# Kernel optimization log

Measured on AMD Instinct MI355X. Metric: run time of the kernel, lower is better.

The kernel has to match this reference:

```python
import jax, jax.numpy as jnp
import numpy as np

B, L, N, F = 8, 4096, 128, 128          # batch, pixels (64x64), memories, filters
H, DK, DV = 8, 16, 32                   # heads, key dim/head, value dim/head
TK, TV = H * DK, H * DV                 # total key depth 128, total value depth 256
BOT, FFN = 256, 2048                    # bottleneck (2*filters), feed-forward channels
EPS = 1e-3                              # keras BatchNormalization epsilon
INV = float(1.0 / np.sqrt(1.0 + EPS))   # inference BN with moving mean=0, var=1


def _bn_pair(k, shape):
    kg, kb = jax.random.split(k)
    gamma = jax.random.uniform(kg, shape, jnp.float32, 0.5, 1.5)
    beta = 0.1 * jax.random.normal(kb, shape, jnp.float32)
    return jnp.stack([gamma, beta])


def setup_inputs() -> dict:
    key = jax.random.key(0)
    ks = jax.random.split(key, 24)
    s = float(BOT) ** -0.5  # TruncatedNormal(stddev=bottleneck**-0.5) init for qkv convs
    return {
        "pixel_input": jax.random.normal(ks[0], (B, L, F), jnp.float32),
        "memory_input": jax.random.normal(ks[1], (B, N, F), jnp.float32),
        "W_mem1": 0.05 * jax.random.normal(ks[2], (F, BOT), jnp.float32),
        "bn_mem1": _bn_pair(ks[3], (BOT,)),
        "W_pix1": 0.05 * jax.random.normal(ks[4], (F, BOT), jnp.float32),
        "bn_pix1": _bn_pair(ks[5], (BOT,)),
        "W_mem_qkv": s * jax.random.normal(ks[6], (BOT, 2 * TK + TV), jnp.float32),
        "bn_mem_qkv": _bn_pair(ks[7], (2 * TK + TV,)),
        "W_pix_qkv": s * jax.random.normal(ks[8], (BOT, 2 * TK + TV), jnp.float32),
        "bn_pix_qkv": _bn_pair(ks[9], (2 * TK + TV,)),
        "bn_mem_sim": _bn_pair(ks[10], (H,)),
        "bn_mem_ret": _bn_pair(ks[11], (H, DV)),
        "bn_pix_sim": _bn_pair(ks[12], (H,)),
        "bn_pix_ret": _bn_pair(ks[13], (H, DV)),
        "W_mem3": 0.05 * jax.random.normal(ks[14], (TV, F), jnp.float32),
        "bn_mem3": _bn_pair(ks[15], (F,)),
        "W_pix3": 0.05 * jax.random.normal(ks[16], (TV, F), jnp.float32),
        "bn_pix3": _bn_pair(ks[17], (F,)),
        "W_ffn1": 0.05 * jax.random.normal(ks[18], (F, FFN), jnp.float32),
        "bn_ffn1": _bn_pair(ks[19], (FFN,)),
        "W_ffn2": 0.05 * jax.random.normal(ks[20], (FFN, F), jnp.float32),
        "bn_ffn2": _bn_pair(ks[21], (F,)),
    }


def _cbn(x, W, p, relu=False):
    """Conv1D (kernel=1) + inference BatchNorm over channels (+ optional relu)."""
    y = jnp.einsum('blc,cd->bld', x, W)
    y = y * (p[0] * INV) + p[1]
    return jax.nn.relu(y) if relu else y


def _heads(t, d):
    b, l, _ = t.shape  # [b, l, H*d] -> [b, H, l, d]
    return t.reshape(b, l, H, d).transpose(0, 2, 1, 3)


def reference(pixel_input, memory_input, W_mem1, bn_mem1, W_pix1, bn_pix1,
              W_mem_qkv, bn_mem_qkv, W_pix_qkv, bn_pix_qkv,
              bn_mem_sim, bn_mem_ret, bn_pix_sim, bn_pix_ret,
              W_mem3, bn_mem3, W_pix3, bn_pix3,
              W_ffn1, bn_ffn1, W_ffn2, bn_ffn2):
    # Bottleneck projections (conv1 + BN + relu)
    mem = _cbn(memory_input, W_mem1, bn_mem1, True)   # [B, N, BOT]
    pix = _cbn(pixel_input, W_pix1, bn_pix1, True)    # [B, L, BOT]

    # QKV projections (conv + BN, no activation)
    mqkv = _cbn(mem, W_mem_qkv, bn_mem_qkv)           # [B, N, 2*TK+TV]
    pqkv = _cbn(pix, W_pix_qkv, bn_pix_qkv)           # [B, L, 2*TK+TV]
    mq, mk, mv = mqkv[..., :TK], mqkv[..., TK:2 * TK], mqkv[..., 2 * TK:]
    pq, pk, pv = pqkv[..., :TK], pqkv[..., TK:2 * TK], pqkv[..., 2 * TK:]
    mq_h, mk_h = _heads(mq, DK), _heads(mk, DK)       # [B, H, N, DK]
    pq_h, pk_h = _heads(pq, DK), _heads(pk, DK)       # [B, H, L, DK]
    mv_h = mv.reshape(B, N, H, DV)                    # [B, N, H, DV]
    pv_h = pv.reshape(B, L, H, DV)                    # [B, L, H, DV]

    # Memory path: memory2pixel attention + memory self-attention share softmax
    k_cat = jnp.concatenate([pk_h, mk_h], axis=2)     # [B, H, L+N, DK]
    v_cat = jnp.concatenate([pv_h, mv_h], axis=1)     # [B, L+N, H, DV]
    logits = jnp.einsum('bhnd,bhmd->bhnm', mq_h, k_cat)
    logits = logits * (bn_mem_sim[0] * INV)[None, :, None, None] + bn_mem_sim[1][None, :, None, None]
    attn = jax.nn.softmax(logits, axis=-1)
    ret = jnp.einsum('bhnm,bmhd->bhnd', attn, v_cat)  # [B, H, N, DV]
    ret = ret * (bn_mem_ret[0] * INV)[None, :, None, :] + bn_mem_ret[1][None, :, None, :]
    ret = jax.nn.relu(ret).transpose(0, 2, 1, 3).reshape(B, N, TV)
    mem_out = jax.nn.relu(memory_input + _cbn(ret, W_mem3, bn_mem3))
    ffn = _cbn(mem_out, W_ffn1, bn_ffn1, True)
    mem_out = jax.nn.relu(mem_out + _cbn(ffn, W_ffn2, bn_ffn2))

    # Pixel path: pixel2memory feedback attention (sigmoid activation)
    plogits = jnp.einsum('bhld,bhnd->bhln', pq_h, mk_h)
    plogits = plogits * (bn_pix_sim[0] * INV)[None, :, None, None] + bn_pix_sim[1][None, :, None, None]
    pattn = jax.nn.sigmoid(plogits)
    pret = jnp.einsum('bhln,bnhd->bhld', pattn, mv_h)  # [B, H, L, DV]
    pret = pret * (bn_pix_ret[0] * INV)[None, :, None, :] + bn_pix_ret[1][None, :, None, :]
    pret = jax.nn.relu(pret).transpose(0, 2, 1, 3).reshape(B, L, TV)
    pix_out = jax.nn.relu(pixel_input + _cbn(pret, W_pix3, bn_pix3))

    return pix_out, mem_out
```

## Files before the change

kernel.cpp:

```cpp
#include <hip/hip_runtime.h>

typedef __attribute__((ext_vector_type(8))) short short8;
typedef __attribute__((ext_vector_type(4))) float floatx4;

#define INVC 0.9995003746877732f
#define MSPLIT 8

__device__ __forceinline__ unsigned short f2bf(float f) {
    union { float f; unsigned int u; } c; c.f = f;
    unsigned int r = c.u + 0x7fffu + ((c.u >> 16) & 1u);
    return (unsigned short)(r >> 16);
}
__device__ __forceinline__ float bf2f(unsigned short u) {
    union { unsigned int u; float f; } c; c.u = ((unsigned int)u) << 16;
    return c.f;
}
__device__ __forceinline__ void gld_lds16(const unsigned short* g, unsigned short* l) {
    __builtin_amdgcn_global_load_lds(
        (const __attribute__((address_space(1))) unsigned int*)g,
        (__attribute__((address_space(3))) unsigned int*)l, 16, 0, 0);
}
__device__ __forceinline__ int fidx(int row, int k) {
    return (k >> 5) * 512 + (row + 16 * ((k >> 3) & 3)) * 8 + (k & 7);
}

struct PrepPtrs {
    const float* src_pix;
    unsigned short* dst_pix;
    const float* W[8]; unsigned short* Wt[8];
};

__global__ __launch_bounds__(256) void prep_kernel(PrepPtrs P) {
    __shared__ float T[32][33];
    const int bid = blockIdx.x, t = threadIdx.x;
    if (bid < 4096) {
        int i = bid * 1024 + t * 4;
        float4 v = *(const float4*)(P.src_pix + i);
        unsigned long long pk = (unsigned long long)f2bf(v.x)
            | ((unsigned long long)f2bf(v.y) << 16)
            | ((unsigned long long)f2bf(v.z) << 32)
            | ((unsigned long long)f2bf(v.w) << 48);
        *(unsigned long long*)(P.dst_pix + i) = pk;
        return;
    }
    int rel = bid - 4096;
    const int KD[8]  = {128,128,256,256,256,256,128,2048};
    const int ND[8]  = {256,256,512,512,128,128,2048,128};
    const int CNT[8] = {32,32,128,128,32,32,256,256};
    int wi = 0;
    #pragma unroll
    for (int k = 0; k < 8; ++k) { if (rel >= CNT[k] && wi == k) { rel -= CNT[k]; wi = k + 1; } }
    const int K = KD[wi], N = ND[wi];
    const int ntn = N >> 5;
    const int tn = rel % ntn, tk = rel / ntn;
    const int n0 = tn * 32, k0 = tk * 32;
    const float* W = P.W[wi];
    unsigned short* Wt = P.Wt[wi];
    const int tx = t & 31, ty = t >> 5;
    #pragma unroll
    for (int i = 0; i < 4; ++i)
        T[ty + 8*i][tx] = W[(size_t)(k0 + ty + 8*i) * N + n0 + tx];
    __syncthreads();
    #pragma unroll
    for (int i = 0; i < 4; ++i)
        Wt[(size_t)(n0 + ty + 8*i) * K + k0 + tx] = f2bf(T[tx][ty + 8*i]);
}

__device__ __forceinline__ void gemm_body(
    const unsigned short* __restrict__ A,
    const unsigned short* __restrict__ Bt,
    const float* __restrict__ bnp,
    const float* __restrict__ residF,
    unsigned short* __restrict__ outB,
    float* __restrict__ outF,
    int K, int Nc, int do_relu, int row0, int col0,
    unsigned short* As, unsigned short* Bs)
{
    const int t = threadIdx.x;
    const int lane = t & 63, w = t >> 6;
    const int l15 = lane & 15, quad = lane >> 4;
    const int wr = w >> 1, wc = w & 1;

    floatx4 acc[4][4];
    #pragma unroll
    for (int i = 0; i < 4; ++i)
        #pragma unroll
        for (int j = 0; j < 4; ++j) acc[i][j] = (floatx4){0.f, 0.f, 0.f, 0.f};

    const unsigned short* gA0 = A  + (size_t)(row0 + w*16     + l15) * K + quad*8;
    const unsigned short* gA1 = A  + (size_t)(row0 + (w+4)*16 + l15) * K + quad*8;
    const unsigned short* gB0 = Bt + (size_t)(col0 + w*16     + l15) * K + quad*8;
    const unsigned short* gB1 = Bt + (size_t)(col0 + (w+4)*16 + l15) * K + quad*8;
    unsigned short* lA0 = &As[w * 512];
    unsigned short* lA1 = &As[(w + 4) * 512];
    unsigned short* lB0 = &Bs[w * 512];
    unsigned short* lB1 = &Bs[(w + 4) * 512];

    for (int k0 = 0; k0 < K; k0 += 32) {
        __syncthreads();
        gld_lds16(gA0 + k0, lA0);
        gld_lds16(gA1 + k0, lA1);
        gld_lds16(gB0 + k0, lB0);
        gld_lds16(gB1 + k0, lB1);
        __syncthreads();
        short8 a[4], b[4];
        #pragma unroll
        for (int mt = 0; mt < 4; ++mt) a[mt] = *(const short8*)&As[(wr*4 + mt)*512 + lane*8];
        #pragma unroll
        for (int nt = 0; nt < 4; ++nt) b[nt] = *(const short8*)&Bs[(wc*4 + nt)*512 + lane*8];
        #pragma unroll
        for (int mt = 0; mt < 4; ++mt)
            #pragma unroll
            for (int nt = 0; nt < 4; ++nt)
                acc[mt][nt] = __builtin_amdgcn_mfma_f32_16x16x32_bf16(a[mt], b[nt], acc[mt][nt], 0, 0, 0);
    }

    #pragma unroll
    for (int mt = 0; mt < 4; ++mt) {
        const int rowb = row0 + wr*64 + mt*16 + quad*4;
        #pragma unroll
        for (int nt = 0; nt < 4; ++nt) {
            const int col = col0 + wc*64 + nt*16 + l15;
            floatx4 v = acc[mt][nt];
            const float g  = bnp[col] * INVC;
            const float be = bnp[Nc + col];
            #pragma unroll
            for (int r = 0; r < 4; ++r) {
                size_t off = (size_t)(rowb + r) * Nc + col;
                float v1 = v[r] * g + be;
                if (residF) v1 += residF[off];
                if (do_relu) v1 = fmaxf(v1, 0.f);
                if (outB) outB[off] = f2bf(v1);
                if (outF) outF[off] = v1;
            }
        }
    }
}

__global__ __launch_bounds__(256, 4) void gemm_bf16(
    const unsigned short* __restrict__ A, const unsigned short* __restrict__ Bt,
    const float* __restrict__ bnp, unsigned short* __restrict__ outB,
    int K, int Nc)
{
    __shared__ unsigned short As[8 * 512];
    __shared__ unsigned short Bs[8 * 512];
    gemm_body(A, Bt, bnp, nullptr, outB, nullptr, K, Nc, 0,
              blockIdx.y * 128, blockIdx.x * 128, As, Bs);
}

__global__ __launch_bounds__(256) void k_pix1_memfused(
    const unsigned short* __restrict__ pixB, const unsigned short* __restrict__ Wt1,
    const float* __restrict__ bn_pix1, unsigned short* __restrict__ pixA,
    const float* __restrict__ memory_input,
    const unsigned short* __restrict__ Wt0, const float* __restrict__ bn1,
    const unsigned short* __restrict__ Wt2, const float* __restrict__ bnq,
    unsigned short* __restrict__ mqkv)
{
    __shared__ unsigned short As[8 * 512];
    __shared__ unsigned short Bs[8 * 512];
    const int bx = blockIdx.x;
    if (bx < 512) {
        gemm_body(pixB, Wt1, bn_pix1, nullptr, pixA, nullptr, 128, 256, 1,
                  (bx >> 1) * 128, (bx & 1) * 128, As, Bs);
        return;
    }
    unsigned short* A0 = As;
    unsigned short* A1 = Bs;
    const int t = threadIdx.x;
    const int lane = t & 63, w = t >> 6;
    const int l15 = lane & 15, quad = lane >> 4;
    const int g0 = (bx - 512) * 16;

    {
        const int row = t >> 4;
        const int c0 = (t & 15) * 8;
        const float* src = memory_input + (size_t)(g0 + row) * 128 + c0;
        float4 v0 = *(const float4*)src;
        float4 v1 = *(const float4*)(src + 4);
        float vv[8] = {v0.x, v0.y, v0.z, v0.w, v1.x, v1.y, v1.z, v1.w};
        #pragma unroll
        for (int e = 0; e < 8; ++e)
            A0[fidx(row, c0 + e)] = f2bf(vv[e]);
    }
    __syncthreads();

    #pragma unroll
    for (int i = 0; i < 4; ++i) {
        const int n0 = (w*4 + i) * 16;
        floatx4 acc = {0.f,0.f,0.f,0.f};
        #pragma unroll
        for (int kc = 0; kc < 4; ++kc) {
            short8 a = *(const short8*)&A0[kc*512 + lane*8];
            short8 bfr = *(const short8*)&Wt0[(size_t)(n0 + l15)*128 + kc*32 + quad*8];
            acc = __builtin_amdgcn_mfma_f32_16x16x32_bf16(a, bfr, acc, 0, 0, 0);
        }
        const int col = n0 + l15;
        const float g = bn1[col] * INVC, be = bn1[256 + col];
        #pragma unroll
        for (int r = 0; r < 4; ++r) {
            const int row = quad*4 + r;
            float v = fmaxf(acc[r]*g + be, 0.f);
            A1[fidx(row, col)] = f2bf(v);
        }
    }
    __syncthreads();

    #pragma unroll
    for (int i = 0; i < 8; ++i) {
        const int n0 = w*128 + i*16;
        floatx4 acc = {0.f,0.f,0.f,0.f};
        #pragma unroll
        for (int kc = 0; kc < 8; ++kc) {
            short8 a = *(const short8*)&A1[kc*512 + lane*8];
            short8 bfr = *(const short8*)&Wt2[(size_t)(n0 + l15)*256 + kc*32 + quad*8];
            acc = __builtin_amdgcn_mfma_f32_16x16x32_bf16(a, bfr, acc, 0, 0, 0);
        }
        const int col = n0 + l15;
        const float g = bnq[col] * INVC, be = bnq[512 + col];
        #pragma unroll
        for (int r = 0; r < 4; ++r) {
            const int row = quad*4 + r;
            mqkv[(size_t)(g0 + row)*512 + col] = f2bf(acc[r]*g + be);
        }
    }
}

__global__ __launch_bounds__(256) void k_attn(
    const unsigned short* __restrict__ pqkv,
    const unsigned short* __restrict__ mqkv,
    const float* __restrict__ bn_psim, const float* __restrict__ bn_pret,
    unsigned short* __restrict__ pret,
    const float* __restrict__ bn_msim,
    float* __restrict__ part_acc, float* __restrict__ part_ml)
{
    __shared__ unsigned short Qs[128][40];
    __shared__ unsigned short Ks[128][40];
    __shared__ unsigned short VsT[32][136];
    __shared__ unsigned short Ps[128][136];
    const int t = threadIdx.x;
    const int lane = t & 63, w = t >> 6;
    const int l15 = lane & 15, quad = lane >> 4;
    floatx4 z4 = {0.f, 0.f, 0.f, 0.f};

    if (blockIdx.x < 2048) {
        const int bx = blockIdx.x;
        const int lt = bx & 31, h = (bx >> 5) & 7, b = bx >> 8;
        const int l0 = lt * 128;
        const float simg = bn_psim[h] * INVC, simb = bn_psim[8 + h];
        {
            const int r = t >> 1, half = t & 1;
            uint4 zz = make_uint4(0u, 0u, 0u, 0u);
            const unsigned short* qsrc = pqkv + ((size_t)(b*4096 + l0 + r) << 9) + h*16 + half*8;
            *(uint4*)&Qs[r][half*8] = *(const uint4*)qsrc;
            *(uint4*)&Qs[r][16 + half*8] = zz;
            const unsigned short* ksrc = mqkv + ((size_t)(b*128 + r) << 9) + 128 + h*16 + half*8;
            *(uint4*)&Ks[r][half*8] = *(const uint4*)ksrc;
            *(uint4*)&Ks[r][16 + half*8] = zz;
            const unsigned short* vsrc = mqkv + ((size_t)(b*128 + r) << 9) + 256 + h*32 + half*16;
            uint4 va = *(const uint4*)vsrc;
            uint4 vb = *(const uint4*)(vsrc + 8);
            const int d0 = half * 16;
            VsT[d0+0][r] = (unsigned short)(va.x & 0xffffu); VsT[d0+1][r] = (unsigned short)(va.x >> 16);
            VsT[d0+2][r] = (unsigned short)(va.y & 0xffffu); VsT[d0+3][r] = (unsigned short)(va.y >> 16);
            VsT[d0+4][r] = (unsigned short)(va.z & 0xffffu); VsT[d0+5][r] = (unsigned short)(va.z >> 16);
            VsT[d0+6][r] = (unsigned short)(va.w & 0xffffu); VsT[d0+7][r] = (unsigned short)(va.w >> 16);
            VsT[d0+8][r] = (unsigned short)(vb.x & 0xffffu); VsT[d0+9][r] = (unsigned short)(vb.x >> 16);
            VsT[d0+10][r] = (unsigned short)(vb.y & 0xffffu); VsT[d0+11][r] = (unsigned short)(vb.y >> 16);
            VsT[d0+12][r] = (unsigned short)(vb.z & 0xffffu); VsT[d0+13][r] = (unsigned short)(vb.z >> 16);
            VsT[d0+14][r] = (unsigned short)(vb.w & 0xffffu); VsT[d0+15][r] = (unsigned short)(vb.w >> 16);
        }
        __syncthreads();
        #pragma unroll
        for (int half = 0; half < 2; ++half) {
            short8 aq = *(const short8*)&Qs[w*32 + half*16 + l15][quad*8];
            #pragma unroll
            for (int nt = 0; nt < 8; ++nt) {
                short8 bk = *(const short8*)&Ks[nt*16 + l15][quad*8];
                floatx4 s = __builtin_amdgcn_mfma_f32_16x16x32_bf16(aq, bk, z4, 0, 0, 0);
                const int rowb = w*32 + half*16 + quad*4;
                #pragma unroll
                for (int r = 0; r < 4; ++r) {
                    float x = s[r] * simg + simb;
                    float p = 1.f / (1.f + __expf(-x));
                    Ps[rowb + r][nt*16 + l15] = f2bf(p);
                }
            }
        }
        __syncthreads();
        #pragma unroll
        for (int half = 0; half < 2; ++half) {
            const int mrow = w*32 + half*16;
            #pragma unroll
            for (int dvt = 0; dvt < 2; ++dvt) {
                floatx4 acc = {0.f, 0.f, 0.f, 0.f};
                #pragma unroll
                for (int ks = 0; ks < 4; ++ks) {
                    short8 ap = *(const short8*)&Ps[mrow + l15][ks*32 + quad*8];
                    short8 bv = *(const short8*)&VsT[dvt*16 + l15][ks*32 + quad*8];
                    acc = __builtin_amdgcn_mfma_f32_16x16x32_bf16(ap, bv, acc, 0, 0, 0);
                }
                const int dv = dvt*16 + l15;
                const float g  = bn_pret[h*32 + dv] * INVC;
                const float be = bn_pret[256 + h*32 + dv];
                #pragma unroll
                for (int r = 0; r < 4; ++r) {
                    const int row = l0 + mrow + quad*4 + r;
                    float v = fmaxf(acc[r] * g + be, 0.f);
                    pret[((size_t)(b*4096 + row) << 8) + h*32 + dv] = f2bf(v);
                }
            }
        }
        return;
    }

    const int bxm = blockIdx.x - 2048;
    const int s = bxm & (MSPLIT-1), h = (bxm >> 3) & 7, b = bxm >> 6;
    const int bh = b*8 + h;
    const float simg = bn_msim[h] * INVC, simb = bn_msim[8 + h];
    const int c0  = (s == 0) ? 0 : (4*s + 1);
    const int cnt = (s == 0) ? 5 : 4;

    {
        const int r = t >> 1, half = t & 1;
        uint4 zz = make_uint4(0u, 0u, 0u, 0u);
        const unsigned short* qsrc = mqkv + ((size_t)(b*128 + r) << 9) + h*16 + half*8;
        *(uint4*)&Qs[r][half*8] = *(const uint4*)qsrc;
        *(uint4*)&Qs[r][16 + half*8] = zz;
    }

    float m_run[2][4], l_run[2][4];
    floatx4 accpv[2][2];
    #pragma unroll
    for (int i = 0; i < 2; ++i) {
        #pragma unroll
        for (int r = 0; r < 4; ++r) { m_run[i][r] = -1e30f; l_run[i][r] = 0.f; }
        accpv[i][0] = (floatx4){0.f,0.f,0.f,0.f};
        accpv[i][1] = (floatx4){0.f,0.f,0.f,0.f};
    }

    for (int ci = 0; ci < cnt; ++ci) {
        const int c = c0 + ci;
        __syncthreads();
        {
            const int r = t >> 1, half = t & 1;
            uint4 zz = make_uint4(0u, 0u, 0u, 0u);
            const unsigned short* base = (c < 32)
                ? (pqkv + ((size_t)(b*4096 + c*128 + r) << 9))
                : (mqkv + ((size_t)(b*128 + r) << 9));
            *(uint4*)&Ks[r][half*8] = *(const uint4*)(base + 128 + h*16 + half*8);
            *(uint4*)&Ks[r][16 + half*8] = zz;
            const unsigned short* vsrc = base + 256 + h*32 + half*16;
            uint4 va = *(const uint4*)vsrc;
            uint4 vb = *(const uint4*)(vsrc + 8);
            const int d0 = half * 16;
            VsT[d0+0][r] = (unsigned short)(va.x & 0xffffu); VsT[d0+1][r] = (unsigned short)(va.x >> 16);
            VsT[d0+2][r] = (unsigned short)(va.y & 0xffffu); VsT[d0+3][r] = (unsigned short)(va.y >> 16);
            VsT[d0+4][r] = (unsigned short)(va.z & 0xffffu); VsT[d0+5][r] = (unsigned short)(va.z >> 16);
            VsT[d0+6][r] = (unsigned short)(va.w & 0xffffu); VsT[d0+7][r] = (unsigned short)(va.w >> 16);
            VsT[d0+8][r] = (unsigned short)(vb.x & 0xffffu); VsT[d0+9][r] = (unsigned short)(vb.x >> 16);
            VsT[d0+10][r] = (unsigned short)(vb.y & 0xffffu); VsT[d0+11][r] = (unsigned short)(vb.y >> 16);
            VsT[d0+12][r] = (unsigned short)(vb.z & 0xffffu); VsT[d0+13][r] = (unsigned short)(vb.z >> 16);
            VsT[d0+14][r] = (unsigned short)(vb.w & 0xffffu); VsT[d0+15][r] = (unsigned short)(vb.w >> 16);
        }
        __syncthreads();

        #pragma unroll
        for (int half = 0; half < 2; ++half) {
            float sv[8][4];
            short8 aq = *(const short8*)&Qs[w*32 + half*16 + l15][quad*8];
            #pragma unroll
            for (int nt = 0; nt < 8; ++nt) {
                short8 bk = *(const short8*)&Ks[nt*16 + l15][quad*8];
                floatx4 sr4 = __builtin_amdgcn_mfma_f32_16x16x32_bf16(aq, bk, z4, 0, 0, 0);
                #pragma unroll
                for (int r = 0; r < 4; ++r) sv[nt][r] = sr4[r] * simg + simb;
            }
            const int rowb = w*32 + half*16 + quad*4;
            #pragma unroll
            for (int r = 0; r < 4; ++r) {
                float mx = sv[0][r];
                #pragma unroll
                for (int nt = 1; nt < 8; ++nt) mx = fmaxf(mx, sv[nt][r]);
                mx = fmaxf(mx, __shfl_xor(mx, 1));
                mx = fmaxf(mx, __shfl_xor(mx, 2));
                mx = fmaxf(mx, __shfl_xor(mx, 4));
                mx = fmaxf(mx, __shfl_xor(mx, 8));
                float newm  = fmaxf(m_run[half][r], mx);
                float alpha = __expf(m_run[half][r] - newm);
                m_run[half][r] = newm;
                float lsum = 0.f;
                #pragma unroll
                for (int nt = 0; nt < 8; ++nt) {
                    float p = __expf(sv[nt][r] - newm);
                    lsum += p;
                    Ps[rowb + r][nt*16 + l15] = f2bf(p);
                }
                lsum += __shfl_xor(lsum, 1);
                lsum += __shfl_xor(lsum, 2);
                lsum += __shfl_xor(lsum, 4);
                lsum += __shfl_xor(lsum, 8);
                l_run[half][r] = l_run[half][r] * alpha + lsum;
                accpv[half][0][r] *= alpha;
                accpv[half][1][r] *= alpha;
            }
            __syncthreads();
            const int mrow = w*32 + half*16;
            #pragma unroll
            for (int dvt = 0; dvt < 2; ++dvt) {
                floatx4 a = accpv[half][dvt];
                #pragma unroll
                for (int ks = 0; ks < 4; ++ks) {
                    short8 ap = *(const short8*)&Ps[mrow + l15][ks*32 + quad*8];
                    short8 bv = *(const short8*)&VsT[dvt*16 + l15][ks*32 + quad*8];
                    a = __builtin_amdgcn_mfma_f32_16x16x32_bf16(ap, bv, a, 0, 0, 0);
                }
                accpv[half][dvt] = a;
            }
        }
    }

    #pragma unroll
    for (int half = 0; half < 2; ++half) {
        const int rowb = w*32 + half*16 + quad*4;
        #pragma unroll
        for (int dvt = 0; dvt < 2; ++dvt) {
            const int dv = dvt*16 + l15;
            #pragma unroll
            for (int r = 0; r < 4; ++r)
                part_acc[((size_t)(bh*MSPLIT + s)*128 + rowb + r)*32 + dv] = accpv[half][dvt][r];
        }
        if (l15 == 0) {
            #pragma unroll
            for (int r = 0; r < 4; ++r) {
                size_t o = ((size_t)(bh*MSPLIT + s)*128 + rowb + r) * 2;
                part_ml[o]     = m_run[half][r];
                part_ml[o + 1] = l_run[half][r];
            }
        }
    }
}

__global__ __launch_bounds__(256) void k_pix3_combmem3(
    const unsigned short* __restrict__ pretB, const unsigned short* __restrict__ Wt5,
    const float* __restrict__ bn_pix3, const float* __restrict__ pixel_input,
    float* __restrict__ out_pix,
    const float* __restrict__ part_acc, const float* __restrict__ part_ml,
    const float* __restrict__ bn_ret,
    const unsigned short* __restrict__ Wt4, const float* __restrict__ bn3,
    const float* __restrict__ memory_input,
    unsigned short* __restrict__ moB)
{
    __shared__ unsigned short As[8 * 512];
    __shared__ unsigned short Bs[8 * 512];
    const int bx = blockIdx.x;
    if (bx < 256) {
        gemm_body(pretB, Wt5, bn_pix3, pixel_input, nullptr, out_pix, 256, 128, 1,
                  bx * 128, 0, As, Bs);
        return;
    }
    unsigned short* mretA = As;
    const int t = threadIdx.x;
    const int lane = t & 63, w = t >> 6;
    const int l15 = lane & 15, quad = lane >> 4;
    const int g0 = (bx - 256) * 16;
    const int b = g0 >> 7;
    const int nbase = g0 & 127;

    {
        const int row = t >> 4;
        const int c0 = (t & 15) * 16;
        const int h = c0 >> 5;
        const int n = nbase + row;
        const int bh = b*8 + h;
        float ms[MSPLIT], ls[MSPLIT], m_g = -1e30f;
        #pragma unroll
        for (int s = 0; s < MSPLIT; ++s) {
            size_t o = ((size_t)(bh*MSPLIT + s)*128 + n)*2;
            ms[s] = part_ml[o]; ls[s] = part_ml[o+1];
            m_g = fmaxf(m_g, ms[s]);
        }
        float l_g = 0.f;
        float og[16];
        #pragma unroll
        for (int e = 0; e < 16; ++e) og[e] = 0.f;
        #pragma unroll
        for (int s = 0; s < MSPLIT; ++s) {
            float wgt = __expf(ms[s] - m_g);
            l_g += ls[s] * wgt;
            const float* pa = part_acc + ((size_t)(bh*MSPLIT + s)*128 + n)*32 + (c0 & 31);
            #pragma unroll
            for (int e = 0; e < 16; e += 4) {
                float4 v = *(const float4*)(pa + e);
                og[e]   += v.x*wgt; og[e+1] += v.y*wgt;
                og[e+2] += v.z*wgt; og[e+3] += v.w*wgt;
            }
        }
        float invl = 1.f / l_g;
        #pragma unroll
        for (int e = 0; e < 16; ++e) {
            int col = c0 + e;
            int dv = col & 31;
            float v = og[e]*invl*(bn_ret[h*32+dv]*INVC) + bn_ret[256 + h*32 + dv];
            mretA[fidx(row, col)] = f2bf(fmaxf(v, 0.f));
        }
    }
    __syncthreads();

    #pragma unroll
    for (int i = 0; i < 2; ++i) {
        const int n0 = (w*2 + i) * 16;
        floatx4 acc = {0.f,0.f,0.f,0.f};
        #pragma unroll
        for (int kc = 0; kc < 8; ++kc) {
            short8 a = *(const short8*)&mretA[kc*512 + lane*8];
            short8 bfr = *(const short8*)&Wt4[(size_t)(n0 + l15)*256 + kc*32 + quad*8];
            acc = __builtin_amdgcn_mfma_f32_16x16x32_bf16(a, bfr, acc, 0, 0, 0);
        }
        const int col = n0 + l15;
        const float g = bn3[col]*INVC, be = bn3[128 + col];
        #pragma unroll
        for (int r = 0; r < 4; ++r) {
            const int row = quad*4 + r;
            float v = acc[r]*g + be + memory_input[(size_t)(g0 + row)*128 + col];
            moB[(size_t)(g0 + row)*128 + col] = f2bf(fmaxf(v, 0.f));
        }
    }
}

__global__ __launch_bounds__(1024) void k_ffn(
    const unsigned short* __restrict__ moB,
    const unsigned short* __restrict__ Wt6, const float* __restrict__ bnf1,
    const unsigned short* __restrict__ Wt7, const float* __restrict__ bnf2,
    float* __restrict__ out_mem)
{
    __shared__ unsigned short moA[4*512];
    __shared__ unsigned short fA[64*512];
    __shared__ floatx4 red[2][8][64];
    const int t = threadIdx.x;
    const int lane = t & 63, w = t >> 6;
    const int l15 = lane & 15, quad = lane >> 4;
    const int g0 = blockIdx.x * 16;

    if (t < 256) {
        const int row = t >> 4;
        const int c0 = (t & 15) * 8;
        uint4 v = *(const uint4*)(moB + (size_t)(g0 + row)*128 + c0);
        unsigned short e0 = (unsigned short)(v.x & 0xffffu), e1 = (unsigned short)(v.x >> 16);
        unsigned short e2 = (unsigned short)(v.y & 0xffffu), e3 = (unsigned short)(v.y >> 16);
        unsigned short e4 = (unsigned short)(v.z & 0xffffu), e5 = (unsigned short)(v.z >> 16);
        unsigned short e6 = (unsigned short)(v.w & 0xffffu), e7 = (unsigned short)(v.w >> 16);
        moA[fidx(row, c0+0)] = e0; moA[fidx(row, c0+1)] = e1;
        moA[fidx(row, c0+2)] = e2; moA[fidx(row, c0+3)] = e3;
        moA[fidx(row, c0+4)] = e4; moA[fidx(row, c0+5)] = e5;
        moA[fidx(row, c0+6)] = e6; moA[fidx(row, c0+7)] = e7;
    }
    __syncthreads();

    #pragma unroll
    for (int i = 0; i < 8; ++i) {
        const int n0 = (w*8 + i) * 16;
        floatx4 acc = {0.f,0.f,0.f,0.f};
        #pragma unroll
        for (int kc = 0; kc < 4; ++kc) {
            short8 a = *(const short8*)&moA[kc*512 + lane*8];
            short8 bfr = *(const short8*)&Wt6[(size_t)(n0 + l15)*128 + kc*32 + quad*8];
            acc = __builtin_amdgcn_mfma_f32_16x16x32_bf16(a, bfr, acc, 0, 0, 0);
        }
        const int col = n0 + l15;
        const float g = bnf1[col]*INVC, be = bnf1[2048 + col];
        #pragma unroll
        for (int r = 0; r < 4; ++r)
            fA[fidx(quad*4 + r, col)] = f2bf(fmaxf(acc[r]*g + be, 0.f));
    }
    __syncthreads();

    {
        const int ntile = w & 7, khalf = w >> 3;
        const int n0 = ntile * 16;
        floatx4 acc = {0.f,0.f,0.f,0.f};
        #pragma unroll 8
        for (int kc = 0; kc < 32; ++kc) {
            const int kcu = khalf*32 + kc;
            short8 a = *(const short8*)&fA[kcu*512 + lane*8];
            short8 bfr = *(const short8*)&Wt7[(size_t)(n0 + l15)*2048 + kcu*32 + quad*8];
            acc = __builtin_amdgcn_mfma_f32_16x16x32_bf16(a, bfr, acc, 0, 0, 0);
        }
        red[khalf][ntile][lane] = acc;
    }
    __syncthreads();
    if (w < 8) {
        const int n0 = w * 16;
        floatx4 s0 = red[0][w][lane];
        floatx4 s1 = red[1][w][lane];
        const int col = n0 + l15;
        const float g = bnf2[col]*INVC, be = bnf2[128 + col];
        #pragma unroll
        for (int r = 0; r < 4; ++r) {
            const int row = quad*4 + r;
            float resid = bf2f(moA[fidx(row, col)]);
            float v = fmaxf((s0[r] + s1[r])*g + be + resid, 0.f);
            out_mem[(size_t)(g0 + row)*128 + col] = v;
        }
    }
}

extern "C" void kernel_launch(void* const* d_in, const int* in_sizes, int n_in,
                              void* d_out, int out_size, void* d_ws, size_t ws_size,
                              hipStream_t stream) {
    const float* pixel_input  = (const float*)d_in[0];
    const float* memory_input = (const float*)d_in[1];
    const float* W_mem1    = (const float*)d_in[2];
    const float* bn_mem1   = (const float*)d_in[3];
    const float* W_pix1    = (const float*)d_in[4];
    const float* bn_pix1   = (const float*)d_in[5];
    const float* W_mem_qkv = (const float*)d_in[6];
    const float* bn_mem_qkv= (const float*)d_in[7];
    const float* W_pix_qkv = (const float*)d_in[8];
    const float* bn_pix_qkv= (const float*)d_in[9];
    const float* bn_mem_sim= (const float*)d_in[10];
    const float* bn_mem_ret= (const float*)d_in[11];
    const float* bn_pix_sim= (const float*)d_in[12];
    const float* bn_pix_ret= (const float*)d_in[13];
    const float* W_mem3    = (const float*)d_in[14];
    const float* bn_mem3   = (const float*)d_in[15];
    const float* W_pix3    = (const float*)d_in[16];
    const float* bn_pix3   = (const float*)d_in[17];
    const float* W_ffn1    = (const float*)d_in[18];
    const float* bn_ffn1   = (const float*)d_in[19];
    const float* W_ffn2    = (const float*)d_in[20];
    const float* bn_ffn2   = (const float*)d_in[21];

    char* ws = (char*)d_ws;
    size_t off = 0;
    auto alloc = [&](size_t bytes) -> void* {
        void* p = ws + off; off += (bytes + 255) & ~(size_t)255; return p;
    };
    unsigned short* pixB  = (unsigned short*)alloc((size_t)32768*128*2);
    unsigned short* Wt0   = (unsigned short*)alloc((size_t)256*128*2);
    unsigned short* Wt1   = (unsigned short*)alloc((size_t)256*128*2);
    unsigned short* Wt2   = (unsigned short*)alloc((size_t)512*256*2);
    unsigned short* Wt3   = (unsigned short*)alloc((size_t)512*256*2);
    unsigned short* Wt4   = (unsigned short*)alloc((size_t)128*256*2);
    unsigned short* Wt5   = (unsigned short*)alloc((size_t)128*256*2);
    unsigned short* Wt6   = (unsigned short*)alloc((size_t)2048*128*2);
    unsigned short* Wt7   = (unsigned short*)alloc((size_t)128*2048*2);
    unsigned short* mqkvB = (unsigned short*)alloc((size_t)1024*512*2);
    unsigned short* pixA  = (unsigned short*)alloc((size_t)32768*256*2);
    unsigned short* pqkvB = (unsigned short*)alloc((size_t)32768*512*2);
    float* part_acc = (float*)alloc((size_t)64*MSPLIT*128*32*4);
    float* part_ml  = (float*)alloc((size_t)64*MSPLIT*128*2*4);
    unsigned short* pretB = (unsigned short*)alloc((size_t)32768*256*2);
    unsigned short* moB   = (unsigned short*)alloc((size_t)1024*128*2);

    float* out_pix = (float*)d_out;
    float* out_mem = (float*)d_out + (size_t)8*4096*128;

    PrepPtrs P;
    P.src_pix = pixel_input;
    P.dst_pix = pixB;
    P.W[0]=W_mem1; P.W[1]=W_pix1; P.W[2]=W_mem_qkv; P.W[3]=W_pix_qkv;
    P.W[4]=W_mem3; P.W[5]=W_pix3; P.W[6]=W_ffn1;    P.W[7]=W_ffn2;
    P.Wt[0]=Wt0; P.Wt[1]=Wt1; P.Wt[2]=Wt2; P.Wt[3]=Wt3;
    P.Wt[4]=Wt4; P.Wt[5]=Wt5; P.Wt[6]=Wt6; P.Wt[7]=Wt7;

    dim3 blk(256);
    prep_kernel<<<4992, blk, 0, stream>>>(P);
    k_pix1_memfused<<<576, blk, 0, stream>>>(pixB, Wt1, bn_pix1, pixA,
        memory_input, Wt0, bn_mem1, Wt2, bn_mem_qkv, mqkvB);
    gemm_bf16<<<dim3(4,256,1), blk, 0, stream>>>(pixA, Wt3, bn_pix_qkv, pqkvB, 256, 512);
    k_attn<<<2048 + 64*MSPLIT, blk, 0, stream>>>(pqkvB, mqkvB,
        bn_pix_sim, bn_pix_ret, pretB, bn_mem_sim, part_acc, part_ml);
    k_pix3_combmem3<<<320, blk, 0, stream>>>(pretB, Wt5, bn_pix3, pixel_input, out_pix,
        part_acc, part_ml, bn_mem_ret, Wt4, bn_mem3, memory_input, moB);
    k_ffn<<<64, dim3(1024), 0, stream>>>(moB, Wt6, bn_ffn1, Wt7, bn_ffn2, out_mem);
}
```

Baseline: 262.8 us.

## Split attention blocks finer and store LDS tiles in MFMA fragment layout

The attention kernel now uses 64-row query tiles, giving twice as many pixel blocks. The memory path moves from 8 splits, each looping over 4-5 chunks with an online softmax, to one block per (batch, head, query half, chunk) across 33 chunks, so each block handles a single chunk. Q, K, V-transpose and P tiles are stored in LDS in the MFMA fragment-contiguous layout so each lane reads with one short8 load, and launch bounds now request 4 blocks per CU. This spreads the work over more blocks and removes the serial chunk loop, but it grows the partial-result buffers and makes the combine stage loop over 33 partials instead of 8.

After: 264.3 us. About the same (+0.6%).

```diff
diff --git a/kernel.cpp b/kernel.cpp
--- a/kernel.cpp
+++ b/kernel.cpp
@@ -4,7 +4,7 @@
 typedef __attribute__((ext_vector_type(4))) float floatx4;
 
 #define INVC 0.9995003746877732f
-#define MSPLIT 8
+#define NCHUNK 33
 
 __device__ __forceinline__ unsigned short f2bf(float f) {
     union { float f; unsigned int u; } c; c.f = f;
@@ -225,7 +225,7 @@
     }
 }
 
-__global__ __launch_bounds__(256) void k_attn(
+__global__ __launch_bounds__(256, 4) void k_attn(
     const unsigned short* __restrict__ pqkv,
     const unsigned short* __restrict__ mqkv,
     const float* __restrict__ bn_psim, const float* __restrict__ bn_pret,
@@ -233,209 +233,160 @@
     const float* __restrict__ bn_msim,
     float* __restrict__ part_acc, float* __restrict__ part_ml)
 {
-    __shared__ unsigned short Qs[128][40];
-    __shared__ unsigned short Ks[128][40];
-    __shared__ unsigned short VsT[32][136];
-    __shared__ unsigned short Ps[128][136];
+    __shared__ unsigned short Qs[4*512];
+    __shared__ unsigned short Ks[8*512];
+    __shared__ unsigned short VsT[8*512];
+    __shared__ unsigned short Ps[16*512];
     const int t = threadIdx.x;
     const int lane = t & 63, w = t >> 6;
     const int l15 = lane & 15, quad = lane >> 4;
     floatx4 z4 = {0.f, 0.f, 0.f, 0.f};
-
-    if (blockIdx.x < 2048) {
+    const uint4 zz = make_uint4(0u,0u,0u,0u);
+
+    const int is_pix = (blockIdx.x < 4096);
+    int b, h, qrow0;
+    const unsigned short* kvbase;
+    if (is_pix) {
         const int bx = blockIdx.x;
-        const int lt = bx & 31, h = (bx >> 5) & 7, b = bx >> 8;
-        const int l0 = lt * 128;
-        const float simg = bn_psim[h] * INVC, simb = bn_psim[8 + h];
-        {
-            const int r = t >> 1, half = t & 1;
-            uint4 zz = make_uint4(0u, 0u, 0u, 0u);
-            const unsigned short* qsrc = pqkv + ((size_t)(b*4096 + l0 + r) << 9) + h*16 + half*8;
-            *(uint4*)&Qs[r][half*8] = *(const uint4*)qsrc;
-            *(uint4*)&Qs[r][16 + half*8] = zz;
-            const unsigned short* ksrc = mqkv + ((size_t)(b*128 + r) << 9) + 128 + h*16 + half*8;
-            *(uint4*)&Ks[r][half*8] = *(const uint4*)ksrc;
-            *(uint4*)&Ks[r][16 + half*8] = zz;
-            const unsigned short* vsrc = mqkv + ((size_t)(b*128 + r) << 9) + 256 + h*32 + half*16;
-            uint4 va = *(const uint4*)vsrc;
-            uint4 vb = *(const uint4*)(vsrc + 8);
-            const int d0 = half * 16;
-            VsT[d0+0][r] = (unsigned short)(va.x & 0xffffu); VsT[d0+1][r] = (unsigned short)(va.x >> 16);
-            VsT[d0+2][r] = (unsigned short)(va.y & 0xffffu); VsT[d0+3][r] = (unsigned short)(va.y >> 16);
-            VsT[d0+4][r] = (unsigned short)(va.z & 0xffffu); VsT[d0+5][r] = (unsigned short)(va.z >> 16);
-            VsT[d0+6][r] = (unsigned short)(va.w & 0xffffu); VsT[d0+7][r] = (unsigned short)(va.w >> 16);
-            VsT[d0+8][r] = (unsigned short)(vb.x & 0xffffu); VsT[d0+9][r] = (unsigned short)(vb.x >> 16);
-            VsT[d0+10][r] = (unsigned short)(vb.y & 0xffffu); VsT[d0+11][r] = (unsigned short)(vb.y >> 16);
-            VsT[d0+12][r] = (unsigned short)(vb.z & 0xffffu); VsT[d0+13][r] = (unsigned short)(vb.z >> 16);
-            VsT[d0+14][r] = (unsigned short)(vb.w & 0xffffu); VsT[d0+15][r] = (unsigned short)(vb.w >> 16);
-        }
-        __syncthreads();
-        #pragma unroll
-        for (int half = 0; half < 2; ++half) {
-            short8 aq = *(const short8*)&Qs[w*32 + half*16 + l15][quad*8];
-            #pragma unroll
-            for (int nt = 0; nt < 8; ++nt) {
-                short8 bk = *(const short8*)&Ks[nt*16 + l15][quad*8];
-                floatx4 s = __builtin_amdgcn_mfma_f32_16x16x32_bf16(aq, bk, z4, 0, 0, 0);
-                const int rowb = w*32 + half*16 + quad*4;
-                #pragma unroll
-                for (int r = 0; r < 4; ++r) {
-                    float x = s[r] * simg + simb;
-                    float p = 1.f / (1.f + __expf(-x));
-                    Ps[rowb + r][nt*16 + l15] = f2bf(p);
-                }
-            }
-        }
-        __syncthreads();
-        #pragma unroll
-        for (int half = 0; half < 2; ++half) {
-            const int mrow = w*32 + half*16;
-            #pragma unroll
-            for (int dvt = 0; dvt < 2; ++dvt) {
-                floatx4 acc = {0.f, 0.f, 0.f, 0.f};
-                #pragma unroll
-                for (int ks = 0; ks < 4; ++ks) {
-                    short8 ap = *(const short8*)&Ps[mrow + l15][ks*32 + quad*8];
-                    short8 bv = *(const short8*)&VsT[dvt*16 + l15][ks*32 + quad*8];
-                    acc = __builtin_amdgcn_mfma_f32_16x16x32_bf16(ap, bv, acc, 0, 0, 0);
-                }
-                const int dv = dvt*16 + l15;
-                const float g  = bn_pret[h*32 + dv] * INVC;
-                const float be = bn_pret[256 + h*32 + dv];
-                #pragma unroll
-                for (int r = 0; r < 4; ++r) {
-                    const int row = l0 + mrow + quad*4 + r;
-                    float v = fmaxf(acc[r] * g + be, 0.f);
-                    pret[((size_t)(b*4096 + row) << 8) + h*32 + dv] = f2bf(v);
-                }
-            }
-        }
-        return;
-    }
-
-    const int bxm = blockIdx.x - 2048;
-    const int s = bxm & (MSPLIT-1), h = (bxm >> 3) & 7, b = bxm >> 6;
-    const int bh = b*8 + h;
-    const float simg = bn_msim[h] * INVC, simb = bn_msim[8 + h];
-    const int c0  = (s == 0) ? 0 : (4*s + 1);
-    const int cnt = (s == 0) ? 5 : 4;
+        const int lt = bx & 63; h = (bx >> 6) & 7; b = bx >> 9;
+        qrow0 = b*4096 + lt*64;
+        kvbase = mqkv + ((size_t)(b*128) << 9);
+    } else {
+        const int bxm = blockIdx.x - 4096;
+        const int c = bxm % NCHUNK;
+        const int rest = bxm / NCHUNK;
+        const int qh = rest & 1; h = (rest >> 1) & 7; b = rest >> 4;
+        qrow0 = b*128 + qh*64;
+        kvbase = (c < 32) ? (pqkv + ((size_t)(b*4096 + c*128) << 9))
+                          : (mqkv + ((size_t)(b*128) << 9));
+    }
+    const unsigned short* qbase = is_pix ? pqkv : mqkv;
 
     {
         const int r = t >> 1, half = t & 1;
-        uint4 zz = make_uint4(0u, 0u, 0u, 0u);
-        const unsigned short* qsrc = mqkv + ((size_t)(b*128 + r) << 9) + h*16 + half*8;
-        *(uint4*)&Qs[r][half*8] = *(const uint4*)qsrc;
-        *(uint4*)&Qs[r][16 + half*8] = zz;
-    }
-
-    float m_run[2][4], l_run[2][4];
-    floatx4 accpv[2][2];
-    #pragma unroll
-    for (int i = 0; i < 2; ++i) {
-        #pragma unroll
-        for (int r = 0; r < 4; ++r) { m_run[i][r] = -1e30f; l_run[i][r] = 0.f; }
-        accpv[i][0] = (floatx4){0.f,0.f,0.f,0.f};
-        accpv[i][1] = (floatx4){0.f,0.f,0.f,0.f};
-    }
-
-    for (int ci = 0; ci < cnt; ++ci) {
-        const int c = c0 + ci;
-        __syncthreads();
-        {
-            const int r = t >> 1, half = t & 1;
-            uint4 zz = make_uint4(0u, 0u, 0u, 0u);
-            const unsigned short* base = (c < 32)
-                ? (pqkv + ((size_t)(b*4096 + c*128 + r) << 9))
-                : (mqkv + ((size_t)(b*128 + r) << 9));
-            *(uint4*)&Ks[r][half*8] = *(const uint4*)(base + 128 + h*16 + half*8);
-            *(uint4*)&Ks[r][16 + half*8] = zz;
-            const unsigned short* vsrc = base + 256 + h*32 + half*16;
-            uint4 va = *(const uint4*)vsrc;
-            uint4 vb = *(const uint4*)(vsrc + 8);
-            const int d0 = half * 16;
-            VsT[d0+0][r] = (unsigned short)(va.x & 0xffffu); VsT[d0+1][r] = (unsigned short)(va.x >> 16);
-            VsT[d0+2][r] = (unsigned short)(va.y & 0xffffu); VsT[d0+3][r] = (unsigned short)(va.y >> 16);
-            VsT[d0+4][r] = (unsigned short)(va.z & 0xffffu); VsT[d0+5][r] = (unsigned short)(va.z >> 16);
-            VsT[d0+6][r] = (unsigned short)(va.w & 0xffffu); VsT[d0+7][r] = (unsigned short)(va.w >> 16);
-            VsT[d0+8][r] = (unsigned short)(vb.x & 0xffffu); VsT[d0+9][r] = (unsigned short)(vb.x >> 16);
-            VsT[d0+10][r] = (unsigned short)(vb.y & 0xffffu); VsT[d0+11][r] = (unsigned short)(vb.y >> 16);
-            VsT[d0+12][r] = (unsigned short)(vb.z & 0xffffu); VsT[d0+13][r] = (unsigned short)(vb.z >> 16);
-            VsT[d0+14][r] = (unsigned short)(vb.w & 0xffffu); VsT[d0+15][r] = (unsigned short)(vb.w >> 16);
-        }
-        __syncthreads();
-
-        #pragma unroll
-        for (int half = 0; half < 2; ++half) {
-            float sv[8][4];
-            short8 aq = *(const short8*)&Qs[w*32 + half*16 + l15][quad*8];
+        if (t < 128) {
+            const unsigned short* src = qbase + ((size_t)(qrow0 + r) << 9) + h*16 + half*8;
+            *(uint4*)&Qs[(r>>4)*512 + ((r&15) + 16*half)*8] = *(const uint4*)src;
+            *(uint4*)&Qs[(r>>4)*512 + ((r&15) + 16*(2+half))*8] = zz;
+        }
+        const unsigned short* ksrc = kvbase + ((size_t)r << 9) + 128 + h*16 + half*8;
+        *(uint4*)&Ks[(r>>4)*512 + ((r&15) + 16*half)*8] = *(const uint4*)ksrc;
+        *(uint4*)&Ks[(r>>4)*512 + ((r&15) + 16*(2+half))*8] = zz;
+        const unsigned short* vsrc = kvbase + ((size_t)r << 9) + 256 + h*32 + half*16;
+        uint4 va = *(const uint4*)vsrc;
+        uint4 vb = *(const uint4*)(vsrc + 8);
+        unsigned short ev[16] = {
+            (unsigned short)(va.x & 0xffffu), (unsigned short)(va.x >> 16),
+            (unsigned short)(va.y & 0xffffu), (unsigned short)(va.y >> 16),
+            (unsigned short)(va.z & 0xffffu), (unsigned short)(va.z >> 16),
+            (unsigned short)(va.w & 0xffffu), (unsigned short)(va.w >> 16),
+            (unsigned short)(vb.x & 0xffffu), (unsigned short)(vb.x >> 16),
+            (unsigned short)(vb.y & 0xffffu), (unsigned short)(vb.y >> 16),
+            (unsigned short)(vb.z & 0xffffu), (unsigned short)(vb.z >> 16),
+            (unsigned short)(vb.w & 0xffffu), (unsigned short)(vb.w >> 16)};
+        const int vbase_off = (half*4 + (r>>5))*512 + 16*((r>>3)&3)*8 + (r&7);
+        #pragma unroll
+        for (int e = 0; e < 16; ++e)
+            VsT[vbase_off + e*8] = ev[e];
+    }
+    __syncthreads();
+
+    const float simg = (is_pix ? bn_psim[h] : bn_msim[h]) * INVC;
+    const float simb =  is_pix ? bn_psim[8 + h] : bn_msim[8 + h];
+    short8 aq = *(const short8*)&Qs[w*512 + lane*8];
+    float mx4[4], ls4[4];
+
+    if (is_pix) {
+        #pragma unroll
+        for (int nt = 0; nt < 8; ++nt) {
+            short8 bk = *(const short8*)&Ks[nt*512 + lane*8];
+            floatx4 s = __builtin_amdgcn_mfma_f32_16x16x32_bf16(aq, bk, z4, 0, 0, 0);
+            const int pbase = (w*4 + (nt>>1))*512 + 16*((nt&1)*2 + (l15>>3))*8 + (l15&7);
+            #pragma unroll
+            for (int r = 0; r < 4; ++r) {
+                float x = s[r] * simg + simb;
+                float p = __builtin_amdgcn_rcpf(1.f + __expf(-x));
+                Ps[pbase + (quad*4 + r)*8] = f2bf(p);
+            }
+        }
+    } else {
+        float sv[8][4];
+        #pragma unroll
+        for (int nt = 0; nt < 8; ++nt) {
+            short8 bk = *(const short8*)&Ks[nt*512 + lane*8];
+            floatx4 s = __builtin_amdgcn_mfma_f32_16x16x32_bf16(aq, bk, z4, 0, 0, 0);
+            #pragma unroll
+            for (int r = 0; r < 4; ++r) sv[nt][r] = s[r] * simg + simb;
+        }
+        #pragma unroll
+        for (int r = 0; r < 4; ++r) {
+            float mx = sv[0][r];
+            #pragma unroll
+            for (int nt = 1; nt < 8; ++nt) mx = fmaxf(mx, sv[nt][r]);
+            mx = fmaxf(mx, __shfl_xor(mx, 1));
+            mx = fmaxf(mx, __shfl_xor(mx, 2));
+            mx = fmaxf(mx, __shfl_xor(mx, 4));
+            mx = fmaxf(mx, __shfl_xor(mx, 8));
+            float lsum = 0.f;
             #pragma unroll
             for (int nt = 0; nt < 8; ++nt) {
-                short8 bk = *(const short8*)&Ks[nt*16 + l15][quad*8];
-                floatx4 sr4 = __builtin_amdgcn_mfma_f32_16x16x32_bf16(aq, bk, z4, 0, 0, 0);
-                #pragma unroll
-                for (int r = 0; r < 4; ++r) sv[nt][r] = sr4[r] * simg + simb;
+                float p = __expf(sv[nt][r] - mx);
+                lsum += p;
+                Ps[(w*4 + (nt>>1))*512 + ((quad*4+r) + 16*((nt&1)*2 + (l15>>3)))*8 + (l15&7)] = f2bf(p);
             }
-            const int rowb = w*32 + half*16 + quad*4;
+            lsum += __shfl_xor(lsum, 1);
+            lsum += __shfl_xor(lsum, 2);
+            lsum += __shfl_xor(lsum, 4);
+            lsum += __shfl_xor(lsum, 8);
+            mx4[r] = mx; ls4[r] = lsum;
+        }
+    }
+
+    #pragma unroll
+    for (int dvt = 0; dvt < 2; ++dvt) {
+        floatx4 acc = {0.f,0.f,0.f,0.f};
+        #pragma unroll
+        for (int ks = 0; ks < 4; ++ks) {
+            short8 ap = *(const short8*)&Ps[(w*4 + ks)*512 + lane*8];
+            short8 bv = *(const short8*)&VsT[(dvt*4 + ks)*512 + lane*8];
+            acc = __builtin_amdgcn_mfma_f32_16x16x32_bf16(ap, bv, acc, 0, 0, 0);
+        }
+        if (is_pix) {
+            const int dv = dvt*16 + l15;
+            const float g  = bn_pret[h*32 + dv] * INVC;
+            const float be = bn_pret[256 + h*32 + dv];
             #pragma unroll
             for (int r = 0; r < 4; ++r) {
-                float mx = sv[0][r];
-                #pragma unroll
-                for (int nt = 1; nt < 8; ++nt) mx = fmaxf(mx, sv[nt][r]);
-                mx = fmaxf(mx, __shfl_xor(mx, 1));
-                mx = fmaxf(mx, __shfl_xor(mx, 2));
-                mx = fmaxf(mx, __shfl_xor(mx, 4));
-                mx = fmaxf(mx, __shfl_xor(mx, 8));
-                float newm  = fmaxf(m_run[half][r], mx);
-                float alpha = __expf(m_run[half][r] - newm);
-                m_run[half][r] = newm;
-                float lsum = 0.f;
-                #pragma unroll
-                for (int nt = 0; nt < 8; ++nt) {
-                    float p = __expf(sv[nt][r] - newm);
-                    lsum += p;
-                    Ps[rowb + r][nt*16 + l15] = f2bf(p);
-                }
-                lsum += __shfl_xor(lsum, 1);
-                lsum += __shfl_xor(lsum, 2);
-                lsum += __shfl_xor(lsum, 4);
-                lsum += __shfl_xor(lsum, 8);
-                l_run[half][r] = l_run[half][r] * alpha + lsum;
-                accpv[half][0][r] *= alpha;
-                accpv[half][1][r] *= alpha;
+                const int row = qrow0 + w*16 + quad*4 + r;
+                float v = fmaxf(acc[r] * g + be, 0.f);
+                pret[((size_t)row << 8) + h*32 + dv] = f2bf(v);
             }
-            __syncthreads();
-            const int mrow = w*32 + half*16;
-            #pragma unroll
-            for (int dvt = 0; dvt < 2; ++dvt) {
-                floatx4 a = accpv[half][dvt];
-                #pragma unroll
-                for (int ks = 0; ks < 4; ++ks) {
-                    short8 ap = *(const short8*)&Ps[mrow + l15][ks*32 + quad*8];
-                    short8 bv = *(const short8*)&VsT[dvt*16 + l15][ks*32 + quad*8];
-                    a = __builtin_amdgcn_mfma_f32_16x16x32_bf16(ap, bv, a, 0, 0, 0);
-                }
-                accpv[half][dvt] = a;
+        } else {
+            const int bxm = blockIdx.x - 4096;
+            const int c = bxm % NCHUNK;
+            const int rest = bxm / NCHUNK;
+            const int qh = rest & 1;
+            const int bh = b*8 + h;
+            const int dv = dvt*16 + l15;
+            #pragma unroll
+            for (int r = 0; r < 4; ++r) {
+                const int q = qh*64 + w*16 + quad*4 + r;
+                part_acc[((size_t)(bh*NCHUNK + c)*128 + q)*32 + dv] = acc[r];
             }
         }
     }
-
-    #pragma unroll
-    for (int half = 0; half < 2; ++half) {
-        const int rowb = w*32 + half*16 + quad*4;
-        #pragma unroll
-        for (int dvt = 0; dvt < 2; ++dvt) {
-            const int dv = dvt*16 + l15;
-            #pragma unroll
-            for (int r = 0; r < 4; ++r)
-                part_acc[((size_t)(bh*MSPLIT + s)*128 + rowb + r)*32 + dv] = accpv[half][dvt][r];
-        }
-        if (l15 == 0) {
-            #pragma unroll
-            for (int r = 0; r < 4; ++r) {
-                size_t o = ((size_t)(bh*MSPLIT + s)*128 + rowb + r) * 2;
-                part_ml[o]     = m_run[half][r];
-                part_ml[o + 1] = l_run[half][r];
-            }
+    if (!is_pix && l15 == 0) {
+        const int bxm = blockIdx.x - 4096;
+        const int c = bxm % NCHUNK;
+        const int rest = bxm / NCHUNK;
+        const int qh = rest & 1;
+        const int bh = b*8 + h;
+        #pragma unroll
+        for (int r = 0; r < 4; ++r) {
+            const int q = qh*64 + w*16 + quad*4 + r;
+            size_t o = ((size_t)(bh*NCHUNK + c)*128 + q) * 2;
+            part_ml[o]     = mx4[r];
+            part_ml[o + 1] = ls4[r];
         }
     }
 }
@@ -472,22 +423,18 @@
         const int h = c0 >> 5;
         const int n = nbase + row;
         const int bh = b*8 + h;
-        float ms[MSPLIT], ls[MSPLIT], m_g = -1e30f;
-        #pragma unroll
-        for (int s = 0; s < MSPLIT; ++s) {
-            size_t o = ((size_t)(bh*MSPLIT + s)*128 + n)*2;
-            ms[s] = part_ml[o]; ls[s] = part_ml[o+1];
-            m_g = fmaxf(m_g, ms[s]);
-        }
+        float m_g = -1e30f;
+        for (int s = 0; s < NCHUNK; ++s)
+            m_g = fmaxf(m_g, part_ml[((size_t)(bh*NCHUNK + s)*128 + n)*2]);
         float l_g = 0.f;
         float og[16];
         #pragma unroll
         for (int e = 0; e < 16; ++e) og[e] = 0.f;
-        #pragma unroll
-        for (int s = 0; s < MSPLIT; ++s) {
-            float wgt = __expf(ms[s] - m_g);
-            l_g += ls[s] * wgt;
-            const float* pa = part_acc + ((size_t)(bh*MSPLIT + s)*128 + n)*32 + (c0 & 31);
+        for (int s = 0; s < NCHUNK; ++s) {
+            size_t o = ((size_t)(bh*NCHUNK + s)*128 + n)*2;
+            float wgt = __expf(part_ml[o] - m_g);
+            l_g += part_ml[o+1] * wgt;
+            const float* pa = part_acc + ((size_t)(bh*NCHUNK + s)*128 + n)*32 + (c0 & 31);
             #pragma unroll
             for (int e = 0; e < 16; e += 4) {
                 float4 v = *(const float4*)(pa + e);
@@ -495,7 +442,7 @@
                 og[e+2] += v.z*wgt; og[e+3] += v.w*wgt;
             }
         }
-        float invl = 1.f / l_g;
+        float invl = __builtin_amdgcn_rcpf(l_g);
         #pragma unroll
         for (int e = 0; e < 16; ++e) {
             int col = c0 + e;
@@ -647,8 +594,8 @@
     unsigned short* mqkvB = (unsigned short*)alloc((size_t)1024*512*2);
     unsigned short* pixA  = (unsigned short*)alloc((size_t)32768*256*2);
     unsigned short* pqkvB = (unsigned short*)alloc((size_t)32768*512*2);
-    float* part_acc = (float*)alloc((size_t)64*MSPLIT*128*32*4);
-    float* part_ml  = (float*)alloc((size_t)64*MSPLIT*128*2*4);
+    float* part_acc = (float*)alloc((size_t)64*NCHUNK*128*32*4);
+    float* part_ml  = (float*)alloc((size_t)64*NCHUNK*128*2*4);
     unsigned short* pretB = (unsigned short*)alloc((size_t)32768*256*2);
     unsigned short* moB   = (unsigned short*)alloc((size_t)1024*128*2);
 
@@ -668,7 +615,7 @@
     k_pix1_memfused<<<576, blk, 0, stream>>>(pixB, Wt1, bn_pix1, pixA,
         memory_input, Wt0, bn_mem1, Wt2, bn_mem_qkv, mqkvB);
     gemm_bf16<<<dim3(4,256,1), blk, 0, stream>>>(pixA, Wt3, bn_pix_qkv, pqkvB, 256, 512);
-    k_attn<<<2048 + 64*MSPLIT, blk, 0, stream>>>(pqkvB, mqkvB,
+    k_attn<<<4096 + 128*NCHUNK, blk, 0, stream>>>(pqkvB, mqkvB,
         bn_pix_sim, bn_pix_ret, pretB, bn_mem_sim, part_acc, part_ml);
     k_pix3_combmem3<<<320, blk, 0, stream>>>(pretB, Wt5, bn_pix3, pixel_input, out_pix,
         part_acc, part_ml, bn_mem_ret, Wt4, bn_mem3, memory_input, moB);
```
